# Optimization experiments

Measured on AMD Instinct MI355X. Metric: run time of the kernel, lower is better.

The kernel has to match this reference:

```python
import jax, jax.numpy as jnp
import numpy as np

N = 50000
E = 800000
IN = 256
C = 64  # hidden_channels
H = 4   # heads
NEG_SLOPE = 0.2


def _rand(key, shape, scale=0.05):
    return jax.random.normal(key, shape, dtype=jnp.float32) * scale


def setup_inputs() -> dict:
    key = jax.random.key(0)
    ks = jax.random.split(key, 32)
    inp = {
        'x': jax.random.normal(ks[0], (N, IN), dtype=jnp.float32),
        'edge_index': jax.random.randint(ks[1], (2, E), 0, N, dtype=jnp.int64),
        'edge_attr': jax.random.uniform(ks[2], (E, 1), dtype=jnp.float32),
    }
    ki = 3
    for l, din in zip((1, 2, 3), (IN, C, C)):
        inp[f'Wl{l}'] = _rand(ks[ki + 0], (din, H * C))
        inp[f'bl{l}'] = jnp.zeros((H * C,), jnp.float32)
        inp[f'Wr{l}'] = _rand(ks[ki + 1], (din, H * C))
        inp[f'br{l}'] = jnp.zeros((H * C,), jnp.float32)
        inp[f'We{l}'] = _rand(ks[ki + 2], (1, H * C))
        inp[f'att{l}'] = _rand(ks[ki + 3], (H, C))
        inp[f'bias{l}'] = jnp.zeros((C,), jnp.float32)
        ki += 4
    inp['prelu_w'] = jnp.full((C,), 0.25, jnp.float32)  # nn.PReLU default init
    return inp


def gatv2_layer(x, src, dst, eattr, Wl, bl, Wr, br, We, att, bias, n):
    h, c = att.shape
    xl = (x @ Wl + bl).reshape(n, h, c)   # source transform
    xr = (x @ Wr + br).reshape(n, h, c)   # destination transform
    ee = (eattr @ We).reshape(-1, h, c)   # edge-feature transform
    m = xl[src] + xr[dst] + ee            # [E', H, C] per-edge messages
    score = jnp.sum(jax.nn.leaky_relu(m, NEG_SLOPE) * att, axis=-1)  # [E', H]
    # segment softmax over destination node neighborhoods (PyG softmax, eps=1e-16)
    mx = jax.ops.segment_max(score, dst, num_segments=n)
    mx = jnp.where(jnp.isfinite(mx), mx, 0.0)
    ex = jnp.exp(score - mx[dst])
    den = jax.ops.segment_sum(ex, dst, num_segments=n)
    alpha = ex / (den[dst] + 1e-16)
    out = jax.ops.segment_sum(alpha[:, :, None] * xl[src], dst, num_segments=n)
    return out.mean(axis=1) + bias        # concat=False -> head mean, then bias


def reference(x, edge_index, edge_attr,
              Wl1, bl1, Wr1, br1, We1, att1, bias1,
              Wl2, bl2, Wr2, br2, We2, att2, bias2,
              Wl3, bl3, Wr3, br3, We3, att3, bias3,
              prelu_w):
    src, dst = edge_index[0], edge_index[1]
    n = x.shape[0]
    # add_self_loops with fill_value='mean': self-loop attr = mean of incoming edge_attr
    cnt = jax.ops.segment_sum(jnp.ones((src.shape[0],), jnp.float32), dst, num_segments=n)
    loop_attr = jax.ops.segment_sum(edge_attr, dst, num_segments=n) / jnp.maximum(cnt, 1.0)[:, None]
    loops = jnp.arange(n, dtype=src.dtype)
    src2 = jnp.concatenate([src, loops])
    dst2 = jnp.concatenate([dst, loops])
    ea2 = jnp.concatenate([edge_attr, loop_attr], axis=0)

    h = gatv2_layer(x, src2, dst2, ea2, Wl1, bl1, Wr1, br1, We1, att1, bias1, n)
    h = gatv2_layer(h, src2, dst2, ea2, Wl2, bl2, Wr2, br2, We2, att2, bias2, n)
    h = gatv2_layer(h, src2, dst2, ea2, Wl3, bl3, Wr3, br3, We3, att3, bias3, n)
    return jnp.where(h >= 0, h, prelu_w * h)  # PReLU per-channel
```

## Files before the change

kernel.cpp:

```cpp
#include <hip/hip_runtime.h>

#define HC 256
#define CCH 64
#define NEG 0.2f

__device__ __forceinline__ float lk(float m) { return m > 0.f ? m : NEG * m; }


__global__ void deg_kernel(const int* __restrict__ dst,
                           const float* __restrict__ eattr,
                           int* __restrict__ cnt, float* __restrict__ sumf, int E) {
  int e = blockIdx.x * blockDim.x + threadIdx.x;
  if (e >= E) return;
  int d = dst[e];
  atomicAdd(&cnt[d], 1);
  atomicAdd(&sumf[d], eattr[e]);
}

__global__ __launch_bounds__(1024)
void scanA(const int* __restrict__ cnt, const float* __restrict__ sumf,
           int* __restrict__ rowptr, float* __restrict__ loopat,
           int* __restrict__ btot, int n) {
  __shared__ int wsum[16];
  int tid = threadIdx.x, lane = tid & 63, w = tid >> 6;
  int i = blockIdx.x * 1024 + tid;
  int v = (i < n) ? cnt[i] : 0;
  int s = v;
  #pragma unroll
  for (int off = 1; off < 64; off <<= 1) {
    int t = __shfl_up(s, off, 64);
    if (lane >= off) s += t;
  }
  if (lane == 63) wsum[w] = s;
  __syncthreads();
  int woff = 0;
  for (int j = 0; j < w; j++) woff += wsum[j];
  if (i < n) {
    rowptr[i] = woff + s - v;
    loopat[i] = sumf[i] / fmaxf((float)v, 1.0f);
  }
  if (tid == 1023) btot[blockIdx.x] = woff + s;
}

__global__ void scanB(const int* __restrict__ btot, int* __restrict__ boff,
                      int* __restrict__ rowptr_n, int nb) {
  int lane = threadIdx.x;
  int v = (lane < nb) ? btot[lane] : 0;
  int s = v;
  #pragma unroll
  for (int off = 1; off < 64; off <<= 1) {
    int t = __shfl_up(s, off, 64);
    if (lane >= off) s += t;
  }
  if (lane < nb) boff[lane] = s - v;
  if (lane == 63) *rowptr_n = s;
}

__global__ void scanC(int* __restrict__ rowptr, const int* __restrict__ boff, int n) {
  int i = blockIdx.x * blockDim.x + threadIdx.x;
  if (i < n) rowptr[i] += boff[i >> 10];
}

__global__ void csr_fill_kernel(const int* __restrict__ src,
                                const int* __restrict__ dst,
                                const float* __restrict__ eattr,
                                const int* __restrict__ rowptr,
                                int* __restrict__ fill,
                                int* __restrict__ csr_src, float* __restrict__ csr_ea, int E) {
  int e = blockIdx.x * blockDim.x + threadIdx.x;
  if (e >= E) return;
  int d = dst[e];
  int p = atomicAdd(&fill[d], 1);
  int slot = rowptr[d] + p;
  csr_src[slot] = src[e];
  csr_ea[slot] = eattr[e];
}


__device__ __forceinline__ void fma8(float a, const float4 blo, const float4 bhi,
                                     float4& c0, float4& c1) {
  c0.x = fmaf(a, blo.x, c0.x); c0.y = fmaf(a, blo.y, c0.y);
  c0.z = fmaf(a, blo.z, c0.z); c0.w = fmaf(a, blo.w, c0.w);
  c1.x = fmaf(a, bhi.x, c1.x); c1.y = fmaf(a, bhi.y, c1.y);
  c1.z = fmaf(a, bhi.z, c1.z); c1.w = fmaf(a, bhi.w, c1.w);
}

__global__ __launch_bounds__(256, 3)
void gemm128(const float* __restrict__ A,
             const float* __restrict__ Wl, const float* __restrict__ bl,
             const float* __restrict__ Wr, const float* __restrict__ br,
             float* __restrict__ xl, float* __restrict__ xr,
             int nrows, int K) {
  __shared__ float As[16][132];
  __shared__ float Ws[16][132];
  const float* W; const float* bb; float* out;
  if (blockIdx.x < 2) { W = Wl; bb = bl; out = xl; }
  else                { W = Wr; bb = br; out = xr; }
  int bn = (blockIdx.x & 1) * 128;
  int bm = blockIdx.y * 128;
  int tid = threadIdx.x;
  int tx = tid & 15, ty = tid >> 4;
  int arow = tid & 127;
  int akk  = (tid >> 7) * 8;
  int wkk  = tid >> 4;
  int wc   = (tid & 15) * 4;

  int row0 = bm + arow;
  bool aval = row0 < nrows;
  const float* arp = A + (size_t)row0 * K + akk;
  const float* wrp = W + (size_t)wkk * HC + bn + wc;

  float4 z = make_float4(0.f, 0.f, 0.f, 0.f);
  float4 a0 = aval ? *(const float4*)arp       : z;
  float4 a1 = aval ? *(const float4*)(arp + 4) : z;
  float4 w0 = *(const float4*)wrp;
  float4 w1 = *(const float4*)(wrp + 64);

  float4 c0[8], c1[8];
  #pragma unroll
  for (int i = 0; i < 8; i++) { c0[i] = z; c1[i] = z; }

  int k0 = 0;
  while (true) {
    As[akk+0][arow] = a0.x; As[akk+1][arow] = a0.y;
    As[akk+2][arow] = a0.z; As[akk+3][arow] = a0.w;
    As[akk+4][arow] = a1.x; As[akk+5][arow] = a1.y;
    As[akk+6][arow] = a1.z; As[akk+7][arow] = a1.w;
    *(float4*)&Ws[wkk][wc]      = w0;
    *(float4*)&Ws[wkk][wc + 64] = w1;
    __syncthreads();
    k0 += 16;
    bool more = k0 < K;
    if (more) {
      a0 = aval ? *(const float4*)(arp + k0)     : z;
      a1 = aval ? *(const float4*)(arp + k0 + 4) : z;
      w0 = *(const float4*)(wrp + (size_t)k0 * HC);
      w1 = *(const float4*)(wrp + (size_t)k0 * HC + 64);
    }
    #pragma unroll
    for (int k = 0; k < 16; k++) {
      float4 alo = *(const float4*)&As[k][ty * 8];
      float4 ahi = *(const float4*)&As[k][ty * 8 + 4];
      float4 blo = *(const float4*)&Ws[k][tx * 4];
      float4 bhi = *(const float4*)&Ws[k][tx * 4 + 64];
      fma8(alo.x, blo, bhi, c0[0], c1[0]);
      fma8(alo.y, blo, bhi, c0[1], c1[1]);
      fma8(alo.z, blo, bhi, c0[2], c1[2]);
      fma8(alo.w, blo, bhi, c0[3], c1[3]);
      fma8(ahi.x, blo, bhi, c0[4], c1[4]);
      fma8(ahi.y, blo, bhi, c0[5], c1[5]);
      fma8(ahi.z, blo, bhi, c0[6], c1[6]);
      fma8(ahi.w, blo, bhi, c0[7], c1[7]);
    }
    if (!more) break;
    __syncthreads();
  }

  float4 bv0 = *(const float4*)(bb + bn + tx * 4);
  float4 bv1 = *(const float4*)(bb + bn + tx * 4 + 64);
  #pragma unroll
  for (int i = 0; i < 8; i++) {
    int row = bm + ty * 8 + i;
    if (row < nrows) {
      float* op = out + (size_t)row * HC + bn + tx * 4;
      float4 o0, o1;
      o0.x = c0[i].x + bv0.x; o0.y = c0[i].y + bv0.y;
      o0.z = c0[i].z + bv0.z; o0.w = c0[i].w + bv0.w;
      o1.x = c1[i].x + bv1.x; o1.y = c1[i].y + bv1.y;
      o1.z = c1[i].z + bv1.z; o1.w = c1[i].w + bv1.w;
      *(float4*)op        = o0;
      *(float4*)(op + 64) = o1;
    }
  }
}


template<int B>
__device__ __forceinline__ void proc_edges(
    const float* __restrict__ xl, int i,
    const int* __restrict__ csr_src, const float* __restrict__ csr_ea,
    const float4 xr4, const float4 we4, const float4 ah4, int l4,
    float& mx, float& den, float4& acc) {
  int sn[B]; float ea[B]; float4 v[B]; float s[B];
  #pragma unroll
  for (int j = 0; j < B; j++) { sn[j] = csr_src[i + j]; ea[j] = csr_ea[i + j]; }
  #pragma unroll
  for (int j = 0; j < B; j++)
    v[j] = *(const float4*)(xl + (size_t)sn[j] * HC + l4);
  #pragma unroll
  for (int j = 0; j < B; j++) {
    float mx_ = fmaf(ea[j], we4.x, v[j].x + xr4.x);
    float my_ = fmaf(ea[j], we4.y, v[j].y + xr4.y);
    float mz_ = fmaf(ea[j], we4.z, v[j].z + xr4.z);
    float mw_ = fmaf(ea[j], we4.w, v[j].w + xr4.w);
    s[j] = lk(mx_) * ah4.x + lk(my_) * ah4.y + lk(mz_) * ah4.z + lk(mw_) * ah4.w;
  }
  #pragma unroll
  for (int off = 8; off >= 1; off >>= 1)
    #pragma unroll
    for (int j = 0; j < B; j++) s[j] += __shfl_xor(s[j], off, 64);
  float bm = s[0];
  #pragma unroll
  for (int j = 1; j < B; j++) bm = fmaxf(bm, s[j]);
  float newm = fmaxf(mx, bm);
  float r = __expf(mx - newm);
  den *= r; acc.x *= r; acc.y *= r; acc.z *= r; acc.w *= r;
  #pragma unroll
  for (int j = 0; j < B; j++) {
    float p = __expf(s[j] - newm);
    den += p;
    acc.x = fmaf(p, v[j].x, acc.x);
    acc.y = fmaf(p, v[j].y, acc.y);
    acc.z = fmaf(p, v[j].z, acc.z);
    acc.w = fmaf(p, v[j].w, acc.w);
  }
  mx = newm;
}

__global__ __launch_bounds__(256)
void gat_edge(const float* __restrict__ xl, const float* __restrict__ xr,
              const float* __restrict__ loopat, const int* __restrict__ rowptr,
              const int* __restrict__ csr_src, const float* __restrict__ csr_ea,
              const float* __restrict__ We, const float* __restrict__ att,
              const float* __restrict__ bias, const float* __restrict__ prelu_w,
              float* __restrict__ out, int n, int is_last) {
  int wv   = threadIdx.x >> 6;
  int node = blockIdx.x * 4 + wv;
  if (node >= n) return;
  int l  = threadIdx.x & 63;
  int l4 = l * 4;
  float4 we4 = *(const float4*)(We + l4);
  float4 ah4 = *(const float4*)(att + l4);
  float4 xr4 = *(const float4*)(xr + (size_t)node * HC + l4);

  float4 vs = *(const float4*)(xl + (size_t)node * HC + l4);
  float la = loopat[node];
  float mx_ = fmaf(la, we4.x, vs.x + xr4.x);
  float my_ = fmaf(la, we4.y, vs.y + xr4.y);
  float mz_ = fmaf(la, we4.z, vs.z + xr4.z);
  float mw_ = fmaf(la, we4.w, vs.w + xr4.w);
  float t = lk(mx_) * ah4.x + lk(my_) * ah4.y + lk(mz_) * ah4.z + lk(mw_) * ah4.w;
  #pragma unroll
  for (int off = 8; off >= 1; off >>= 1) t += __shfl_xor(t, off, 64);
  float mx = t, den = 1.f; float4 acc = vs;

  int beg = rowptr[node], end = rowptr[node + 1];
  int i = beg;
  for (; i + 8 <= end; i += 8)
    proc_edges<8>(xl, i, csr_src, csr_ea, xr4, we4, ah4, l4, mx, den, acc);
  if (i + 4 <= end) {
    proc_edges<4>(xl, i, csr_src, csr_ea, xr4, we4, ah4, l4, mx, den, acc);
    i += 4;
  }
  for (; i < end; i++)
    proc_edges<1>(xl, i, csr_src, csr_ea, xr4, we4, ah4, l4, mx, den, acc);

  float inv = 1.f / (den + 1e-16f);
  float4 a;
  a.x = acc.x * inv; a.y = acc.y * inv; a.z = acc.z * inv; a.w = acc.w * inv;
  a.x += __shfl_xor(a.x, 16, 64); a.x += __shfl_xor(a.x, 32, 64);
  a.y += __shfl_xor(a.y, 16, 64); a.y += __shfl_xor(a.y, 32, 64);
  a.z += __shfl_xor(a.z, 16, 64); a.z += __shfl_xor(a.z, 32, 64);
  a.w += __shfl_xor(a.w, 16, 64); a.w += __shfl_xor(a.w, 32, 64);
  if (l < 16) {
    int c = l * 4;
    float4 bv = *(const float4*)(bias + c);
    float4 o;
    o.x = 0.25f * a.x + bv.x;
    o.y = 0.25f * a.y + bv.y;
    o.z = 0.25f * a.z + bv.z;
    o.w = 0.25f * a.w + bv.w;
    if (is_last) {
      float4 pw = *(const float4*)(prelu_w + c);
      o.x = o.x >= 0.f ? o.x : pw.x * o.x;
      o.y = o.y >= 0.f ? o.y : pw.y * o.y;
      o.z = o.z >= 0.f ? o.z : pw.z * o.z;
      o.w = o.w >= 0.f ? o.w : pw.w * o.w;
    }
    *(float4*)(out + (size_t)node * CCH + c) = o;
  }
}


extern "C" void kernel_launch(void* const* d_in, const int* in_sizes, int n_in,
                              void* d_out, int out_size, void* d_ws, size_t ws_size,
                              hipStream_t stream) {
  const float* x     = (const float*)d_in[0];
  const int*   ei    = (const int*)d_in[1];
  const float* eattr = (const float*)d_in[2];
  int N = in_sizes[0] / HC;
  int E = in_sizes[1] / 2;
  const int* src = ei;
  const int* dst = ei + E;

  const float* Wl[3]  = {(const float*)d_in[3],  (const float*)d_in[10], (const float*)d_in[17]};
  const float* bl[3]  = {(const float*)d_in[4],  (const float*)d_in[11], (const float*)d_in[18]};
  const float* Wr[3]  = {(const float*)d_in[5],  (const float*)d_in[12], (const float*)d_in[19]};
  const float* br[3]  = {(const float*)d_in[6],  (const float*)d_in[13], (const float*)d_in[20]};
  const float* Wev[3] = {(const float*)d_in[7],  (const float*)d_in[14], (const float*)d_in[21]};
  const float* attv[3]= {(const float*)d_in[8],  (const float*)d_in[15], (const float*)d_in[22]};
  const float* bias[3]= {(const float*)d_in[9],  (const float*)d_in[16], (const float*)d_in[23]};
  const float* prelu  = (const float*)d_in[24];

  char* p = (char*)d_ws;
  float* xl     = (float*)p; p += (size_t)N * HC * 4;
  float* xr     = (float*)p; p += (size_t)N * HC * 4;
  float* hbuf   = (float*)p; p += (size_t)N * CCH * 4;
  int*   cnt    = (int*)p;   p += (size_t)N * 4;
  int*   fill   = (int*)p;   p += (size_t)N * 4;
  float* sumf   = (float*)p; p += (size_t)N * 4;
  float* loopat = (float*)p; p += (size_t)N * 4;
  int*   rowptr = (int*)p;   p += (size_t)(N + 8) * 4;
  int*   btot   = (int*)p;   p += 64 * 4;
  int*   boff   = (int*)p;   p += 64 * 4;
  int*   csr_src= (int*)p;   p += (size_t)E * 4;
  float* csr_ea = (float*)p; p += (size_t)E * 4;

  hipMemsetAsync(cnt, 0, (size_t)N * 3 * 4, stream);

  int tb = 256;
  int nb = (N + 1023) / 1024;
  deg_kernel<<<dim3((E + tb - 1) / tb), dim3(tb), 0, stream>>>(dst, eattr, cnt, sumf, E);
  scanA<<<dim3(nb), dim3(1024), 0, stream>>>(cnt, sumf, rowptr, loopat, btot, N);
  scanB<<<dim3(1), dim3(64), 0, stream>>>(btot, boff, rowptr + N, nb);
  scanC<<<dim3((N + tb - 1) / tb), dim3(tb), 0, stream>>>(rowptr, boff, N);
  csr_fill_kernel<<<dim3((E + tb - 1) / tb), dim3(tb), 0, stream>>>(src, dst, eattr, rowptr,
                                                                    fill, csr_src, csr_ea, E);

  const float* in = x;
  int K = 256;
  for (int l = 0; l < 3; l++) {
    dim3 g(4, (N + 127) / 128);
    gemm128<<<g, dim3(256), 0, stream>>>(in, Wl[l], bl[l], Wr[l], br[l], xl, xr, N, K);
    float* o = (l == 2) ? (float*)d_out : hbuf;
    gat_edge<<<dim3((N + 3) / 4), dim3(256), 0, stream>>>(xl, xr, loopat, rowptr,
                                                          csr_src, csr_ea,
                                                          Wev[l], attv[l], bias[l], prelu,
                                                          o, N, l == 2);
    in = hbuf;
    K = CCH;
  }
}
```

Measured before the change: 911.5 us.

## Replace FP32 SIMT GEMM with split-bf16 MFMA GEMM for node transforms

Measured after the change: 900.7 us. No clear change (-1.2%).

```diff
diff --git a/kernel.cpp b/kernel.cpp
--- a/kernel.cpp
+++ b/kernel.cpp
@@ -4,7 +4,18 @@
 #define CCH 64
 #define NEG 0.2f
 
+typedef __attribute__((ext_vector_type(8))) short bf16x8;
+typedef __attribute__((ext_vector_type(4))) float f32x4;
+
 __device__ __forceinline__ float lk(float m) { return m > 0.f ? m : NEG * m; }
+
+__device__ __forceinline__ unsigned bf16rne(float x) {
+  unsigned u = __float_as_uint(x);
+  return (u + 0x7FFFu + ((u >> 16) & 1u)) >> 16;
+}
+__device__ __forceinline__ float bfval(unsigned h) {
+  return __uint_as_float(h << 16);
+}
 
 
 __global__ void deg_kernel(const int* __restrict__ dst,
@@ -77,99 +88,102 @@
 }
 
 
-__device__ __forceinline__ void fma8(float a, const float4 blo, const float4 bhi,
-                                     float4& c0, float4& c1) {
-  c0.x = fmaf(a, blo.x, c0.x); c0.y = fmaf(a, blo.y, c0.y);
-  c0.z = fmaf(a, blo.z, c0.z); c0.w = fmaf(a, blo.w, c0.w);
-  c1.x = fmaf(a, bhi.x, c1.x); c1.y = fmaf(a, bhi.y, c1.y);
-  c1.z = fmaf(a, bhi.z, c1.z); c1.w = fmaf(a, bhi.w, c1.w);
-}
-
-__global__ __launch_bounds__(256, 3)
-void gemm128(const float* __restrict__ A,
-             const float* __restrict__ Wl, const float* __restrict__ bl,
-             const float* __restrict__ Wr, const float* __restrict__ br,
-             float* __restrict__ xl, float* __restrict__ xr,
-             int nrows, int K) {
-  __shared__ float As[16][132];
-  __shared__ float Ws[16][132];
-  const float* W; const float* bb; float* out;
-  if (blockIdx.x < 2) { W = Wl; bb = bl; out = xl; }
-  else                { W = Wr; bb = br; out = xr; }
-  int bn = (blockIdx.x & 1) * 128;
-  int bm = blockIdx.y * 128;
+__global__ void cvtW(const float* __restrict__ W, unsigned short* __restrict__ WTh,
+                     unsigned short* __restrict__ WTl, int K) {
+  int t = blockIdx.x * blockDim.x + threadIdx.x;
+  if (t >= K * 256) return;
+  int k = t >> 8, c = t & 255;
+  float v = W[t];
+  unsigned hb = bf16rne(v);
+  float lo = v - bfval(hb);
+  unsigned lb = bf16rne(lo);
+  WTh[(size_t)c * K + k] = (unsigned short)hb;
+  WTl[(size_t)c * K + k] = (unsigned short)lb;
+}
+
+
+__global__ __launch_bounds__(256, 2)
+void gemm_mfma(const float* __restrict__ A,
+               const unsigned short* __restrict__ WTh_l, const unsigned short* __restrict__ WTl_l,
+               const unsigned short* __restrict__ WTh_r, const unsigned short* __restrict__ WTl_r,
+               const float* __restrict__ bl, const float* __restrict__ br,
+               float* __restrict__ xl, float* __restrict__ xr,
+               int nrows, int K) {
+  __shared__ unsigned short Ahs[64][40];
+  __shared__ unsigned short Als[64][40];
+  const unsigned short *Wh, *Wlo; const float* bb; float* out;
+  if (blockIdx.x == 0) { Wh = WTh_l; Wlo = WTl_l; bb = bl; out = xl; }
+  else                 { Wh = WTh_r; Wlo = WTl_r; bb = br; out = xr; }
+  int bm = blockIdx.y * 64;
   int tid = threadIdx.x;
-  int tx = tid & 15, ty = tid >> 4;
-  int arow = tid & 127;
-  int akk  = (tid >> 7) * 8;
-  int wkk  = tid >> 4;
-  int wc   = (tid & 15) * 4;
-
-  int row0 = bm + arow;
-  bool aval = row0 < nrows;
-  const float* arp = A + (size_t)row0 * K + akk;
-  const float* wrp = W + (size_t)wkk * HC + bn + wc;
-
-  float4 z = make_float4(0.f, 0.f, 0.f, 0.f);
-  float4 a0 = aval ? *(const float4*)arp       : z;
-  float4 a1 = aval ? *(const float4*)(arp + 4) : z;
-  float4 w0 = *(const float4*)wrp;
-  float4 w1 = *(const float4*)(wrp + 64);
-
-  float4 c0[8], c1[8];
-  #pragma unroll
-  for (int i = 0; i < 8; i++) { c0[i] = z; c1[i] = z; }
-
-  int k0 = 0;
-  while (true) {
-    As[akk+0][arow] = a0.x; As[akk+1][arow] = a0.y;
-    As[akk+2][arow] = a0.z; As[akk+3][arow] = a0.w;
-    As[akk+4][arow] = a1.x; As[akk+5][arow] = a1.y;
-    As[akk+6][arow] = a1.z; As[akk+7][arow] = a1.w;
-    *(float4*)&Ws[wkk][wc]      = w0;
-    *(float4*)&Ws[wkk][wc + 64] = w1;
+  int wv = tid >> 6, l = tid & 63;
+  int lrow = l & 15;
+  int lk   = (l >> 4) * 8;
+  int wbase = wv * 64;
+
+  int srow = tid >> 2;
+  int sk   = (tid & 3) * 8;
+  int grow = bm + srow;
+  bool gval = grow < nrows;
+  const float* ap = A + (size_t)grow * K + sk;
+
+  f32x4 acc[4][4] = {};
+
+  for (int k0 = 0; k0 < K; k0 += 32) {
+    float4 z4 = make_float4(0.f, 0.f, 0.f, 0.f);
+    float4 v0 = gval ? *(const float4*)(ap + k0)     : z4;
+    float4 v1 = gval ? *(const float4*)(ap + k0 + 4) : z4;
+    float e_[8] = {v0.x, v0.y, v0.z, v0.w, v1.x, v1.y, v1.z, v1.w};
+    unsigned hh[8], ll[8];
+    #pragma unroll
+    for (int j = 0; j < 8; j++) {
+      hh[j] = bf16rne(e_[j]);
+      float lo = e_[j] - bfval(hh[j]);
+      ll[j] = bf16rne(lo);
+    }
+    uint4 H = make_uint4(hh[0] | (hh[1] << 16), hh[2] | (hh[3] << 16),
+                         hh[4] | (hh[5] << 16), hh[6] | (hh[7] << 16));
+    uint4 L = make_uint4(ll[0] | (ll[1] << 16), ll[2] | (ll[3] << 16),
+                         ll[4] | (ll[5] << 16), ll[6] | (ll[7] << 16));
     __syncthreads();
-    k0 += 16;
-    bool more = k0 < K;
-    if (more) {
-      a0 = aval ? *(const float4*)(arp + k0)     : z;
-      a1 = aval ? *(const float4*)(arp + k0 + 4) : z;
-      w0 = *(const float4*)(wrp + (size_t)k0 * HC);
-      w1 = *(const float4*)(wrp + (size_t)k0 * HC + 64);
-    }
-    #pragma unroll
-    for (int k = 0; k < 16; k++) {
-      float4 alo = *(const float4*)&As[k][ty * 8];
-      float4 ahi = *(const float4*)&As[k][ty * 8 + 4];
-      float4 blo = *(const float4*)&Ws[k][tx * 4];
-      float4 bhi = *(const float4*)&Ws[k][tx * 4 + 64];
-      fma8(alo.x, blo, bhi, c0[0], c1[0]);
-      fma8(alo.y, blo, bhi, c0[1], c1[1]);
-      fma8(alo.z, blo, bhi, c0[2], c1[2]);
-      fma8(alo.w, blo, bhi, c0[3], c1[3]);
-      fma8(ahi.x, blo, bhi, c0[4], c1[4]);
-      fma8(ahi.y, blo, bhi, c0[5], c1[5]);
-      fma8(ahi.z, blo, bhi, c0[6], c1[6]);
-      fma8(ahi.w, blo, bhi, c0[7], c1[7]);
-    }
-    if (!more) break;
+    *(uint4*)&Ahs[srow][sk] = H;
+    *(uint4*)&Als[srow][sk] = L;
     __syncthreads();
-  }
-
-  float4 bv0 = *(const float4*)(bb + bn + tx * 4);
-  float4 bv1 = *(const float4*)(bb + bn + tx * 4 + 64);
-  #pragma unroll
-  for (int i = 0; i < 8; i++) {
-    int row = bm + ty * 8 + i;
-    if (row < nrows) {
-      float* op = out + (size_t)row * HC + bn + tx * 4;
-      float4 o0, o1;
-      o0.x = c0[i].x + bv0.x; o0.y = c0[i].y + bv0.y;
-      o0.z = c0[i].z + bv0.z; o0.w = c0[i].w + bv0.w;
-      o1.x = c1[i].x + bv1.x; o1.y = c1[i].y + bv1.y;
-      o1.z = c1[i].z + bv1.z; o1.w = c1[i].w + bv1.w;
-      *(float4*)op        = o0;
-      *(float4*)(op + 64) = o1;
+
+    bf16x8 ah[4], al[4];
+    #pragma unroll
+    for (int rt = 0; rt < 4; rt++) {
+      ah[rt] = *(const bf16x8*)&Ahs[rt * 16 + lrow][lk];
+      al[rt] = *(const bf16x8*)&Als[rt * 16 + lrow][lk];
+    }
+    #pragma unroll
+    for (int ct = 0; ct < 4; ct++) {
+      size_t wo = (size_t)(wbase + ct * 16 + lrow) * K + k0 + lk;
+      bf16x8 bh = *(const bf16x8*)(Wh + wo);
+      bf16x8 bo = *(const bf16x8*)(Wlo + wo);
+      #pragma unroll
+      for (int rt = 0; rt < 4; rt++) {
+        acc[rt][ct] = __builtin_amdgcn_mfma_f32_16x16x32_bf16(ah[rt], bh, acc[rt][ct], 0, 0, 0);
+        acc[rt][ct] = __builtin_amdgcn_mfma_f32_16x16x32_bf16(ah[rt], bo, acc[rt][ct], 0, 0, 0);
+        acc[rt][ct] = __builtin_amdgcn_mfma_f32_16x16x32_bf16(al[rt], bh, acc[rt][ct], 0, 0, 0);
+      }
+    }
+  }
+
+  int rsub = (l >> 4) * 4;
+  #pragma unroll
+  for (int ct = 0; ct < 4; ct++) {
+    int col = wbase + ct * 16 + lrow;
+    float bv = bb[col];
+    #pragma unroll
+    for (int rt = 0; rt < 4; rt++) {
+      int rbase = bm + rt * 16 + rsub;
+      f32x4 c = acc[rt][ct];
+      #pragma unroll
+      for (int j = 0; j < 4; j++) {
+        int row = rbase + j;
+        if (row < nrows) out[(size_t)row * HC + col] = c[j] + bv;
+      }
     }
   }
 }
@@ -313,6 +327,10 @@
   int*   rowptr = (int*)p;   p += (size_t)(N + 8) * 4;
   int*   btot   = (int*)p;   p += 64 * 4;
   int*   boff   = (int*)p;   p += 64 * 4;
+  unsigned short* wth_l = (unsigned short*)p; p += (size_t)256 * 256 * 2;
+  unsigned short* wtl_l = (unsigned short*)p; p += (size_t)256 * 256 * 2;
+  unsigned short* wth_r = (unsigned short*)p; p += (size_t)256 * 256 * 2;
+  unsigned short* wtl_r = (unsigned short*)p; p += (size_t)256 * 256 * 2;
   int*   csr_src= (int*)p;   p += (size_t)E * 4;
   float* csr_ea = (float*)p; p += (size_t)E * 4;
 
@@ -330,8 +348,11 @@
   const float* in = x;
   int K = 256;
   for (int l = 0; l < 3; l++) {
-    dim3 g(4, (N + 127) / 128);
-    gemm128<<<g, dim3(256), 0, stream>>>(in, Wl[l], bl[l], Wr[l], br[l], xl, xr, N, K);
+    int wels = K * 256;
+    cvtW<<<dim3((wels + tb - 1) / tb), dim3(tb), 0, stream>>>(Wl[l], wth_l, wtl_l, K);
+    cvtW<<<dim3((wels + tb - 1) / tb), dim3(tb), 0, stream>>>(Wr[l], wth_r, wtl_r, K);
+    gemm_mfma<<<dim3(2, (N + 63) / 64), dim3(256), 0, stream>>>(
+        in, wth_l, wtl_l, wth_r, wtl_r, bl[l], br[l], xl, xr, N, K);
     float* o = (l == 2) ? (float*)d_out : hbuf;
     gat_edge<<<dim3((N + 3) / 4), dim3(256), 0, stream>>>(xl, xr, loopat, rowptr,
                                                           csr_src, csr_ea,
```
